# Kernel optimization log

Hardware: AMD Instinct MI355X
Metric: run time of the kernel (lower is better)

## Reference

```python
import jax, jax.numpy as jnp
import numpy as np
import math

D_MODEL = 1024
NHEAD = 16
HEAD_DIM = D_MODEL // NHEAD
SCALE = math.sqrt(HEAD_DIM)
B, TQ, TK = 8, 1024, 1024


def setup_inputs() -> dict:
    key = jax.random.key(0)
    ks = jax.random.split(key, 8)
    init = 0.02
    return {
        "query": jax.random.normal(ks[0], (B, TQ, D_MODEL), jnp.float32),
        "memory": jax.random.normal(ks[1], (B, TK, D_MODEL), jnp.float32),
        "coverage": jax.random.uniform(ks[2], (B, TK), jnp.float32),
        "Wq": jax.random.normal(ks[3], (D_MODEL, D_MODEL), jnp.float32) * init,
        "bq": jnp.zeros((D_MODEL,), jnp.float32),
        "Wk": jax.random.normal(ks[4], (D_MODEL, D_MODEL), jnp.float32) * init,
        "bk": jnp.zeros((D_MODEL,), jnp.float32),
        "Wv": jax.random.normal(ks[5], (D_MODEL, D_MODEL), jnp.float32) * init,
        "bv": jnp.zeros((D_MODEL,), jnp.float32),
        "Wo": jax.random.normal(ks[6], (D_MODEL, D_MODEL), jnp.float32) * init,
        "bo": jnp.zeros((D_MODEL,), jnp.float32),
        "Wcov": jax.random.normal(ks[7], (NHEAD, 1), jnp.float32) * init,
    }


def reference(query, memory, coverage, Wq, bq, Wk, bk, Wv, bv, Wo, bo, Wcov):
    b, tq, _ = query.shape
    tk = memory.shape[1]
    # projections, split into heads: [B, H, T, hd]
    Q = (query @ Wq.T + bq).reshape(b, tq, NHEAD, HEAD_DIM).transpose(0, 2, 1, 3)
    K = (memory @ Wk.T + bk).reshape(b, tk, NHEAD, HEAD_DIM).transpose(0, 2, 1, 3)
    V = (memory @ Wv.T + bv).reshape(b, tk, NHEAD, HEAD_DIM).transpose(0, 2, 1, 3)
    scores = jnp.einsum('bhqd,bhkd->bhqk', Q, K) / SCALE
    # coverage_proj: Linear(1, nhead, bias=False) -> outer product coverage x Wcov[:,0]
    cov_bias = jnp.einsum('bk,h->bhk', coverage, Wcov[:, 0])[:, :, None, :]  # [B,H,1,Tk]
    scores = scores + cov_bias
    attn = jax.nn.softmax(scores, axis=-1)
    # dropout is identity in eval/deterministic mode
    out = jnp.einsum('bhqk,bhkd->bhqd', attn, V).transpose(0, 2, 1, 3).reshape(b, tq, D_MODEL)
    out = out @ Wo.T + bo
    new_coverage = coverage + attn.mean(axis=1).sum(axis=1)  # [B,Tk]
    return out, new_coverage
```

## Files before the change

kernel.cpp:

```cpp
#include <hip/hip_runtime.h>

typedef __bf16 bf16_t;
typedef bf16_t bf16x8 __attribute__((ext_vector_type(8)));
typedef float f32x4 __attribute__((ext_vector_type(4)));

#define MFMA16(a, b, c) __builtin_amdgcn_mfma_f32_16x16x32_bf16(a, b, c, 0, 0, 0)

#define LOG2E 1.44269504f
#define C1 0.18033688f

__device__ inline void async_copy16(const bf16_t* g, bf16_t* l) {
  __builtin_amdgcn_global_load_lds(
      (const __attribute__((address_space(1))) void*)g,
      (__attribute__((address_space(3))) void*)l, 16, 0, 0);
}

__device__ inline bf16x8 lds_frag(const bf16_t* lds, int row, int c8) {
  return *(const bf16x8*)(lds + row * 64 + ((c8 ^ (row & 7)) << 3));
}

template <int NCHUNK, int NT>
__device__ inline void stage_tile(const bf16_t* __restrict__ g, size_t ld,
                                  bf16_t* lds, int tid) {
#pragma unroll
  for (int it = 0; it < NCHUNK / NT; ++it) {
    int f = it * NT + tid;
    int row = f >> 3;
    int c8 = (f & 7) ^ (row & 7);
    async_copy16(g + (size_t)row * ld + c8 * 8, lds + f * 8);
  }
}

__global__ __launch_bounds__(256) void convert_kernel(
    const float* __restrict__ q, const float* __restrict__ mem,
    const float* __restrict__ wq, const float* __restrict__ wk,
    const float* __restrict__ wv, const float* __restrict__ wo, bf16_t* Xq,
    bf16_t* Xm, bf16_t* Wqb, bf16_t* Wkb, bf16_t* Wvb, bf16_t* Wob) {
  size_t i = ((size_t)blockIdx.x * 256 + threadIdx.x) * 8;
  const float* src;
  bf16_t* dst;
  size_t off;
  if (i < 8388608u)        { src = q;   dst = Xq;  off = i; }
  else if (i < 16777216u)  { src = mem; dst = Xm;  off = i - 8388608u; }
  else if (i < 17825792u)  { src = wq;  dst = Wqb; off = i - 16777216u; }
  else if (i < 18874368u)  { src = wk;  dst = Wkb; off = i - 17825792u; }
  else if (i < 19922944u)  { src = wv;  dst = Wvb; off = i - 18874368u; }
  else                     { src = wo;  dst = Wob; off = i - 19922944u; }
  float4 f0 = *(const float4*)(src + off);
  float4 f1 = *(const float4*)(src + off + 4);
  union { bf16_t h[8]; uint4 u; } t;
  t.h[0] = (bf16_t)f0.x; t.h[1] = (bf16_t)f0.y;
  t.h[2] = (bf16_t)f0.z; t.h[3] = (bf16_t)f0.w;
  t.h[4] = (bf16_t)f1.x; t.h[5] = (bf16_t)f1.y;
  t.h[6] = (bf16_t)f1.z; t.h[7] = (bf16_t)f1.w;
  *(uint4*)(dst + off) = t.u;
}

template <int MODE>
__global__ __launch_bounds__(256) void gemm_nt(
    const bf16_t* __restrict__ A, const bf16_t* __restrict__ Bw,
    const float* __restrict__ bias, void* __restrict__ Cout) {
  __shared__ bf16_t As[128 * 64];
  __shared__ bf16_t Bs[128 * 64];
  const int tid = threadIdx.x;
  const int wave = tid >> 6, lane = tid & 63, quad = lane >> 4, c = lane & 15;
  const int wm = (wave & 1) * 64, wn = (wave >> 1) * 64;
  const size_t bm = blockIdx.x, bn = blockIdx.y;
  const bf16_t* Ab = A + bm * 128 * 1024;
  const bf16_t* Bb = Bw + bn * 128 * 1024;
  const f32x4 z4 = {0.f, 0.f, 0.f, 0.f};
  f32x4 acc[4][4];
#pragma unroll
  for (int i = 0; i < 4; ++i)
#pragma unroll
    for (int j = 0; j < 4; ++j) acc[i][j] = z4;

  for (int kt = 0; kt < 16; ++kt) {
    if (kt) __syncthreads();
    stage_tile<1024, 256>(Ab + kt * 64, 1024, As, tid);
    stage_tile<1024, 256>(Bb + kt * 64, 1024, Bs, tid);
    __syncthreads();
#pragma unroll
    for (int ks = 0; ks < 2; ++ks) {
      bf16x8 af[4], bfr[4];
#pragma unroll
      for (int i = 0; i < 4; ++i)
        af[i] = lds_frag(As, wm + 16 * i + c, ks * 4 + quad);
#pragma unroll
      for (int j = 0; j < 4; ++j)
        bfr[j] = lds_frag(Bs, wn + 16 * j + c, ks * 4 + quad);
#pragma unroll
      for (int i = 0; i < 4; ++i)
#pragma unroll
        for (int j = 0; j < 4; ++j)
          acc[i][j] = MFMA16(af[i], bfr[j], acc[i][j]);
    }
  }
#pragma unroll
  for (int i = 0; i < 4; ++i)
#pragma unroll
    for (int j = 0; j < 4; ++j) {
      int gc = (int)bn * 128 + wn + 16 * j + c;
      float bvv = bias[gc];
      if (MODE == 2) {
        int b = (int)(bm >> 3);
        int kk = (int)(bm & 7) * 128 + wm + 16 * i + quad * 4;
        union { bf16_t h4[4]; uint2 u; } pk;
#pragma unroll
        for (int r = 0; r < 4; ++r) pk.h4[r] = (bf16_t)(acc[i][j][r] + bvv);
        *(uint2*)((bf16_t*)Cout + ((size_t)(b * 1024 + gc)) * 1024 + kk) = pk.u;
      } else {
        int gr0 = (int)bm * 128 + wm + 16 * i + quad * 4;
#pragma unroll
        for (int r = 0; r < 4; ++r) {
          float v = acc[i][j][r] + bvv;
          size_t idx = (size_t)(gr0 + r) * 1024 + gc;
          if (MODE == 1)
            ((float*)Cout)[idx] = v;
          else
            ((bf16_t*)Cout)[idx] = (bf16_t)v;
        }
      }
    }
}

__global__ __launch_bounds__(512) void attn_fwd(
    const bf16_t* __restrict__ Qp, const bf16_t* __restrict__ Kp,
    const bf16_t* __restrict__ Vt, const float* __restrict__ coverage,
    const float* __restrict__ Wcov, bf16_t* __restrict__ Hb,
    float* __restrict__ part) {
  __shared__ bf16_t Qs[128 * 64];
  __shared__ bf16_t Ks[64 * 64];
  __shared__ bf16_t Vs[64 * 64];
  __shared__ bf16_t Ps[8][16 * 64];
  __shared__ float covb[1024];
  __shared__ float covsum[1024];
  const int tid = threadIdx.x;
  const int wave = tid >> 6, lane = tid & 63, quad = lane >> 4, c = lane & 15;
  const int qx = blockIdx.x, h = blockIdx.y, b = blockIdx.z;
  const int q0 = qx * 128;
  const float wcl = Wcov[h] * LOG2E;
  const f32x4 z4 = {0.f, 0.f, 0.f, 0.f};

  stage_tile<1024, 512>(Qp + ((size_t)(b * 1024 + q0)) * 1024 + h * 64, 1024,
                        Qs, tid);
  for (int i = tid; i < 1024; i += 512) {
    covb[i] = coverage[b * 1024 + i] * wcl;
    covsum[i] = 0.f;
  }

  float lpart = 0.f;
  f32x4 O[4] = {z4, z4, z4, z4};
  bf16x8 qf0, qf1;
  bf16_t* Pw = &Ps[wave][0];

  for (int kt = 0; kt < 16; ++kt) {
    const int k0 = kt * 64;
    if (kt) __syncthreads();
    stage_tile<512, 512>(Kp + ((size_t)(b * 1024 + k0)) * 1024 + h * 64, 1024,
                         Ks, tid);
    stage_tile<512, 512>(Vt + ((size_t)(b * 1024 + h * 64)) * 1024 + k0, 1024,
                         Vs, tid);
    __syncthreads();
    if (kt == 0) {
      qf0 = lds_frag(Qs, wave * 16 + c, quad);
      qf1 = lds_frag(Qs, wave * 16 + c, 4 + quad);
    }
    f32x4 S[4] = {z4, z4, z4, z4};
#pragma unroll
    for (int j = 0; j < 4; ++j) {
      S[j] = MFMA16(lds_frag(Ks, j * 16 + c, quad), qf0, S[j]);
      S[j] = MFMA16(lds_frag(Ks, j * 16 + c, 4 + quad), qf1, S[j]);
    }
#pragma unroll
    for (int j = 0; j < 4; ++j) {
      f32x4 cb = *(const f32x4*)&covb[k0 + j * 16 + quad * 4];
      union { bf16_t h4[4]; uint2 u; } pk;
#pragma unroll
      for (int r = 0; r < 4; ++r) {
        float p = exp2f(S[j][r] * C1 + cb[r]);
        lpart += p;
        pk.h4[r] = (bf16_t)p;
      }
      int k8 = j * 2 + (quad >> 1);
      *(uint2*)(Pw + c * 64 + ((k8 ^ (c & 7)) << 3) + (quad & 1) * 4) = pk.u;
    }
#pragma unroll
    for (int ks = 0; ks < 2; ++ks) {
      bf16x8 pb =
          *(const bf16x8*)(Pw + c * 64 + (((ks * 4 + quad) ^ (c & 7)) << 3));
#pragma unroll
      for (int j = 0; j < 4; ++j)
        O[j] = MFMA16(lds_frag(Vs, j * 16 + c, ks * 4 + quad), pb, O[j]);
    }
  }

  lpart += __shfl_xor(lpart, 16);
  lpart += __shfl_xor(lpart, 32);
  float linv = 1.f / lpart;

  size_t rowbase = ((size_t)(b * 1024 + q0 + wave * 16 + c)) * 1024 + h * 64;
#pragma unroll
  for (int j = 0; j < 4; ++j) {
    union { bf16_t h4[4]; uint2 u; } pk;
#pragma unroll
    for (int r = 0; r < 4; ++r) pk.h4[r] = (bf16_t)(O[j][r] * linv);
    *(uint2*)(Hb + rowbase + j * 16 + quad * 4) = pk.u;
  }

  float linv_r[4];
#pragma unroll
  for (int r = 0; r < 4; ++r) linv_r[r] = __shfl(linv, quad * 4 + r);

  for (int kt = 0; kt < 16; ++kt) {
    const int k0 = kt * 64;
    __syncthreads();
    stage_tile<512, 512>(Kp + ((size_t)(b * 1024 + k0)) * 1024 + h * 64, 1024,
                         Ks, tid);
    __syncthreads();
    f32x4 S[4] = {z4, z4, z4, z4};
#pragma unroll
    for (int j = 0; j < 4; ++j) {
      S[j] = MFMA16(qf0, lds_frag(Ks, j * 16 + c, quad), S[j]);
      S[j] = MFMA16(qf1, lds_frag(Ks, j * 16 + c, 4 + quad), S[j]);
    }
#pragma unroll
    for (int j = 0; j < 4; ++j) {
      float cb = covb[k0 + j * 16 + c];
      float vsum = 0.f;
#pragma unroll
      for (int r = 0; r < 4; ++r)
        vsum += exp2f(S[j][r] * C1 + cb) * linv_r[r];
      vsum += __shfl_xor(vsum, 16);
      vsum += __shfl_xor(vsum, 32);
      if (quad == 0) atomicAdd(&covsum[k0 + j * 16 + c], vsum);
    }
  }
  __syncthreads();
  float* ps = part + ((size_t)(b * 128 + h * 8 + qx)) * 1024;
  for (int i = tid; i < 1024; i += 512) ps[i] = covsum[i];
}

__global__ __launch_bounds__(256) void cov_reduce(
    const float* __restrict__ part, const float* __restrict__ coverage,
    float* __restrict__ covout) {
  int i = blockIdx.x * 256 + threadIdx.x;
  int b = i >> 10, k = i & 1023;
  const float* p = part + (size_t)b * 128 * 1024 + k;
  float s = 0.f;
  for (int j = 0; j < 128; ++j) s += p[(size_t)j * 1024];
  covout[i] = coverage[i] + s * 0.0625f;
}

extern "C" void kernel_launch(void* const* d_in, const int* in_sizes, int n_in,
                              void* d_out, int out_size, void* d_ws,
                              size_t ws_size, hipStream_t stream) {
  const float* query = (const float*)d_in[0];
  const float* memory = (const float*)d_in[1];
  const float* coverage = (const float*)d_in[2];
  const float* Wq = (const float*)d_in[3];
  const float* bq = (const float*)d_in[4];
  const float* Wk = (const float*)d_in[5];
  const float* bk = (const float*)d_in[6];
  const float* Wv = (const float*)d_in[7];
  const float* bv = (const float*)d_in[8];
  const float* Wo = (const float*)d_in[9];
  const float* bo = (const float*)d_in[10];
  const float* Wcov = (const float*)d_in[11];

  char* w = (char*)d_ws;
  const size_t MB = 1024 * 1024;
  bf16_t* Xq = (bf16_t*)(w + 0);
  bf16_t* Xm = (bf16_t*)(w + 16 * MB);
  bf16_t* Wqb = (bf16_t*)(w + 32 * MB);
  bf16_t* Wkb = (bf16_t*)(w + 34 * MB);
  bf16_t* Wvb = (bf16_t*)(w + 36 * MB);
  bf16_t* Wob = (bf16_t*)(w + 38 * MB);
  bf16_t* Qp = (bf16_t*)(w + 40 * MB);
  bf16_t* Kp = (bf16_t*)(w + 56 * MB);
  bf16_t* Vt = (bf16_t*)(w + 72 * MB);
  bf16_t* Hb = (bf16_t*)(w + 0);
  float* part = (float*)(w + 16 * MB);

  float* out = (float*)d_out;
  float* covout = out + (size_t)8 * 1024 * 1024;

  convert_kernel<<<10240, 256, 0, stream>>>(query, memory, Wq, Wk, Wv, Wo, Xq,
                                            Xm, Wqb, Wkb, Wvb, Wob);
  gemm_nt<0><<<dim3(64, 8), 256, 0, stream>>>(Xq, Wqb, bq, Qp);
  gemm_nt<0><<<dim3(64, 8), 256, 0, stream>>>(Xm, Wkb, bk, Kp);
  gemm_nt<2><<<dim3(64, 8), 256, 0, stream>>>(Xm, Wvb, bv, Vt);
  attn_fwd<<<dim3(8, 16, 8), 512, 0, stream>>>(Qp, Kp, Vt, coverage, Wcov, Hb,
                                               part);
  gemm_nt<1><<<dim3(64, 8), 256, 0, stream>>>(Hb, Wob, bo, out);
  cov_reduce<<<32, 256, 0, stream>>>(part, coverage, covout);
}
```

Before: 360.3 us.

## Fuse QKV GEMMs into one launch, shrink attention blocks, double-buffer coverage pass

Replaces the three separate Q/K/V projection launches with a single gemm_qkv launch over a 24-wide column grid that selects input, bias and output layout per block. The attention kernel moves from 128-query/512-thread blocks to 64-query/256-thread blocks, doubling the grid and the number of coverage partials that cov_reduce sums. The second pass over K double-buffers K tiles in the Ks/Vs buffers so the next tile loads during compute, dropping one barrier per iteration. The aim is better CU occupancy and fewer launches, at the cost of more partial-sum traffic and K reloads per query. Wqkv is assumed to be Wqb, Wkb and Wvb stored contiguously.

```diff
diff --git a/kernel.cpp b/kernel.cpp
--- a/kernel.cpp
+++ b/kernel.cpp
@@ -56,10 +56,78 @@
   *(uint4*)(dst + off) = t.u;
 }
 
-template <int MODE>
-__global__ __launch_bounds__(256) void gemm_nt(
+__global__ __launch_bounds__(256) void gemm_qkv(
+    const bf16_t* __restrict__ Xq, const bf16_t* __restrict__ Xm,
+    const bf16_t* __restrict__ Wqkv, const float* __restrict__ bq,
+    const float* __restrict__ bk, const float* __restrict__ bv,
+    bf16_t* __restrict__ Qp, bf16_t* __restrict__ Kp,
+    bf16_t* __restrict__ Vt) {
+  __shared__ bf16_t As[128 * 64];
+  __shared__ bf16_t Bs[128 * 64];
+  const int tid = threadIdx.x;
+  const int wave = tid >> 6, lane = tid & 63, quad = lane >> 4, c = lane & 15;
+  const int wm = (wave & 1) * 64, wn = (wave >> 1) * 64;
+  const size_t bm = blockIdx.x, bn = blockIdx.y;
+  const int which = (int)(bn >> 3);
+  const bf16_t* A = which ? Xm : Xq;
+  const float* bias = which == 0 ? bq : (which == 1 ? bk : bv);
+  const bf16_t* Ab = A + bm * 128 * 1024;
+  const bf16_t* Bb = Wqkv + bn * 128 * 1024;
+  const f32x4 z4 = {0.f, 0.f, 0.f, 0.f};
+  f32x4 acc[4][4];
+#pragma unroll
+  for (int i = 0; i < 4; ++i)
+#pragma unroll
+    for (int j = 0; j < 4; ++j) acc[i][j] = z4;
+
+  for (int kt = 0; kt < 16; ++kt) {
+    if (kt) __syncthreads();
+    stage_tile<1024, 256>(Ab + kt * 64, 1024, As, tid);
+    stage_tile<1024, 256>(Bb + kt * 64, 1024, Bs, tid);
+    __syncthreads();
+#pragma unroll
+    for (int ks = 0; ks < 2; ++ks) {
+      bf16x8 af[4], bfr[4];
+#pragma unroll
+      for (int i = 0; i < 4; ++i)
+        af[i] = lds_frag(As, wm + 16 * i + c, ks * 4 + quad);
+#pragma unroll
+      for (int j = 0; j < 4; ++j)
+        bfr[j] = lds_frag(Bs, wn + 16 * j + c, ks * 4 + quad);
+#pragma unroll
+      for (int i = 0; i < 4; ++i)
+#pragma unroll
+        for (int j = 0; j < 4; ++j)
+          acc[i][j] = MFMA16(af[i], bfr[j], acc[i][j]);
+    }
+  }
+#pragma unroll
+  for (int i = 0; i < 4; ++i)
+#pragma unroll
+    for (int j = 0; j < 4; ++j) {
+      int gc = (int)bn * 128 + wn + 16 * j + c;
+      int gcl = gc & 1023;
+      float bvv = bias[gcl];
+      if (which == 2) {
+        int b = (int)(bm >> 3);
+        int kk = (int)(bm & 7) * 128 + wm + 16 * i + quad * 4;
+        union { bf16_t h4[4]; uint2 u; } pk;
+#pragma unroll
+        for (int r = 0; r < 4; ++r) pk.h4[r] = (bf16_t)(acc[i][j][r] + bvv);
+        *(uint2*)(Vt + ((size_t)(b * 1024 + gcl)) * 1024 + kk) = pk.u;
+      } else {
+        bf16_t* Cout = which ? Kp : Qp;
+        int gr0 = (int)bm * 128 + wm + 16 * i + quad * 4;
+#pragma unroll
+        for (int r = 0; r < 4; ++r)
+          Cout[(size_t)(gr0 + r) * 1024 + gcl] = (bf16_t)(acc[i][j][r] + bvv);
+      }
+    }
+}
+
+__global__ __launch_bounds__(256) void gemm_out(
     const bf16_t* __restrict__ A, const bf16_t* __restrict__ Bw,
-    const float* __restrict__ bias, void* __restrict__ Cout) {
+    const float* __restrict__ bias, float* __restrict__ Cout) {
   __shared__ bf16_t As[128 * 64];
   __shared__ bf16_t Bs[128 * 64];
   const int tid = threadIdx.x;
@@ -102,49 +170,34 @@
     for (int j = 0; j < 4; ++j) {
       int gc = (int)bn * 128 + wn + 16 * j + c;
       float bvv = bias[gc];
-      if (MODE == 2) {
-        int b = (int)(bm >> 3);
-        int kk = (int)(bm & 7) * 128 + wm + 16 * i + quad * 4;
-        union { bf16_t h4[4]; uint2 u; } pk;
-#pragma unroll
-        for (int r = 0; r < 4; ++r) pk.h4[r] = (bf16_t)(acc[i][j][r] + bvv);
-        *(uint2*)((bf16_t*)Cout + ((size_t)(b * 1024 + gc)) * 1024 + kk) = pk.u;
-      } else {
-        int gr0 = (int)bm * 128 + wm + 16 * i + quad * 4;
-#pragma unroll
-        for (int r = 0; r < 4; ++r) {
-          float v = acc[i][j][r] + bvv;
-          size_t idx = (size_t)(gr0 + r) * 1024 + gc;
-          if (MODE == 1)
-            ((float*)Cout)[idx] = v;
-          else
-            ((bf16_t*)Cout)[idx] = (bf16_t)v;
-        }
-      }
-    }
-}
-
-__global__ __launch_bounds__(512) void attn_fwd(
+      int gr0 = (int)bm * 128 + wm + 16 * i + quad * 4;
+#pragma unroll
+      for (int r = 0; r < 4; ++r)
+        Cout[(size_t)(gr0 + r) * 1024 + gc] = acc[i][j][r] + bvv;
+    }
+}
+
+__global__ __launch_bounds__(256) void attn_fwd(
     const bf16_t* __restrict__ Qp, const bf16_t* __restrict__ Kp,
     const bf16_t* __restrict__ Vt, const float* __restrict__ coverage,
     const float* __restrict__ Wcov, bf16_t* __restrict__ Hb,
     float* __restrict__ part) {
-  __shared__ bf16_t Qs[128 * 64];
+  __shared__ bf16_t Qs[64 * 64];
   __shared__ bf16_t Ks[64 * 64];
   __shared__ bf16_t Vs[64 * 64];
-  __shared__ bf16_t Ps[8][16 * 64];
+  __shared__ bf16_t Ps[4][16 * 64];
   __shared__ float covb[1024];
   __shared__ float covsum[1024];
   const int tid = threadIdx.x;
   const int wave = tid >> 6, lane = tid & 63, quad = lane >> 4, c = lane & 15;
   const int qx = blockIdx.x, h = blockIdx.y, b = blockIdx.z;
-  const int q0 = qx * 128;
+  const int q0 = qx * 64;
   const float wcl = Wcov[h] * LOG2E;
   const f32x4 z4 = {0.f, 0.f, 0.f, 0.f};
 
-  stage_tile<1024, 512>(Qp + ((size_t)(b * 1024 + q0)) * 1024 + h * 64, 1024,
-                        Qs, tid);
-  for (int i = tid; i < 1024; i += 512) {
+  stage_tile<512, 256>(Qp + ((size_t)(b * 1024 + q0)) * 1024 + h * 64, 1024,
+                       Qs, tid);
+  for (int i = tid; i < 1024; i += 256) {
     covb[i] = coverage[b * 1024 + i] * wcl;
     covsum[i] = 0.f;
   }
@@ -157,9 +210,9 @@
   for (int kt = 0; kt < 16; ++kt) {
     const int k0 = kt * 64;
     if (kt) __syncthreads();
-    stage_tile<512, 512>(Kp + ((size_t)(b * 1024 + k0)) * 1024 + h * 64, 1024,
+    stage_tile<512, 256>(Kp + ((size_t)(b * 1024 + k0)) * 1024 + h * 64, 1024,
                          Ks, tid);
-    stage_tile<512, 512>(Vt + ((size_t)(b * 1024 + h * 64)) * 1024 + k0, 1024,
+    stage_tile<512, 256>(Vt + ((size_t)(b * 1024 + h * 64)) * 1024 + k0, 1024,
                          Vs, tid);
     __syncthreads();
     if (kt == 0) {
@@ -212,17 +265,23 @@
 #pragma unroll
   for (int r = 0; r < 4; ++r) linv_r[r] = __shfl(linv, quad * 4 + r);
 
+  __syncthreads();
+  stage_tile<512, 256>(Kp + ((size_t)(b * 1024)) * 1024 + h * 64, 1024, Ks,
+                       tid);
+  __syncthreads();
   for (int kt = 0; kt < 16; ++kt) {
     const int k0 = kt * 64;
-    __syncthreads();
-    stage_tile<512, 512>(Kp + ((size_t)(b * 1024 + k0)) * 1024 + h * 64, 1024,
-                         Ks, tid);
-    __syncthreads();
+    bf16_t* cur = (kt & 1) ? Vs : Ks;
+    if (kt < 15) {
+      bf16_t* nxt = (kt & 1) ? Ks : Vs;
+      stage_tile<512, 256>(
+          Kp + ((size_t)(b * 1024 + k0 + 64)) * 1024 + h * 64, 1024, nxt, tid);
+    }
     f32x4 S[4] = {z4, z4, z4, z4};
 #pragma unroll
     for (int j = 0; j < 4; ++j) {
-      S[j] = MFMA16(qf0, lds_frag(Ks, j * 16 + c, quad), S[j]);
-      S[j] = MFMA16(qf1, lds_frag(Ks, j * 16 + c, 4 + quad), S[j]);
+      S[j] = MFMA16(qf0, lds_frag(cur, j * 16 + c, quad), S[j]);
+      S[j] = MFMA16(qf1, lds_frag(cur, j * 16 + c, 4 + quad), S[j]);
     }
 #pragma unroll
     for (int j = 0; j < 4; ++j) {
@@ -235,10 +294,10 @@
       vsum += __shfl_xor(vsum, 32);
       if (quad == 0) atomicAdd(&covsum[k0 + j * 16 + c], vsum);
     }
-  }
-  __syncthreads();
-  float* ps = part + ((size_t)(b * 128 + h * 8 + qx)) * 1024;
-  for (int i = tid; i < 1024; i += 512) ps[i] = covsum[i];
+    __syncthreads();
+  }
+  float* ps = part + ((size_t)(b * 256 + h * 16 + qx)) * 1024;
+  for (int i = tid; i < 1024; i += 256) ps[i] = covsum[i];
 }
 
 __global__ __launch_bounds__(256) void cov_reduce(
@@ -246,9 +305,9 @@
     float* __restrict__ covout) {
   int i = blockIdx.x * 256 + threadIdx.x;
   int b = i >> 10, k = i & 1023;
-  const float* p = part + (size_t)b * 128 * 1024 + k;
+  const float* p = part + (size_t)b * 256 * 1024 + k;
   float s = 0.f;
-  for (int j = 0; j < 128; ++j) s += p[(size_t)j * 1024];
+  for (int j = 0; j < 256; ++j) s += p[(size_t)j * 1024];
   covout[i] = coverage[i] + s * 0.0625f;
 }
 
@@ -287,11 +346,10 @@
 
   convert_kernel<<<10240, 256, 0, stream>>>(query, memory, Wq, Wk, Wv, Wo, Xq,
                                             Xm, Wqb, Wkb, Wvb, Wob);
-  gemm_nt<0><<<dim3(64, 8), 256, 0, stream>>>(Xq, Wqb, bq, Qp);
-  gemm_nt<0><<<dim3(64, 8), 256, 0, stream>>>(Xm, Wkb, bk, Kp);
-  gemm_nt<2><<<dim3(64, 8), 256, 0, stream>>>(Xm, Wvb, bv, Vt);
-  attn_fwd<<<dim3(8, 16, 8), 512, 0, stream>>>(Qp, Kp, Vt, coverage, Wcov, Hb,
-                                               part);
-  gemm_nt<1><<<dim3(64, 8), 256, 0, stream>>>(Hb, Wob, bo, out);
+  gemm_qkv<<<dim3(64, 24), 256, 0, stream>>>(Xq, Xm, Wqb, bq, bk, bv, Qp, Kp,
+                                             Vt);
+  attn_fwd<<<dim3(16, 16, 8), 256, 0, stream>>>(Qp, Kp, Vt, coverage, Wcov,
+                                                Hb, part);
+  gemm_out<<<dim3(64, 8), 256, 0, stream>>>(Hb, Wob, bo, out);
   cov_reduce<<<32, 256, 0, stream>>>(part, coverage, covout);
 }
```

After: 355.2 us. About the same (-1.4%).
